# Kernel tuning notes

Hardware: AMD Instinct MI355X
Metric: run time of the kernel (lower is better)

## Reference

```python
import jax, jax.numpy as jnp
import numpy as np
import math

C = 256
N_HEAD = 8
GROUPS = 32
EPS = 1e-5


def group_norm(x, scale, bias, groups=GROUPS, eps=EPS):
    # x: [B, C, H, W]
    b, c, h, w = x.shape
    xg = x.reshape(b, groups, c // groups, h, w)
    mean = xg.mean(axis=(2, 3, 4), keepdims=True)
    var = xg.var(axis=(2, 3, 4), keepdims=True)
    xg = (xg - mean) * jax.lax.rsqrt(var + eps)
    x = xg.reshape(b, c, h, w)
    return x * scale[None, :, None, None] + bias[None, :, None, None]


def setup_inputs() -> dict:
    key = jax.random.key(0)
    ks = jax.random.split(key, 8)
    B, H, W = 8, 32, 32
    inp = {
        "input_q": jax.random.normal(ks[0], (B, C, H, W), dtype=jnp.float32),
        "input_kv": jax.random.normal(ks[1], (B, C, H, W), dtype=jnp.float32),
        # GroupNorm affine params (torch default: weight=1, bias=0)
        "gq_scale": jnp.ones((C,), jnp.float32),
        "gq_bias": jnp.zeros((C,), jnp.float32),
        "gkv_scale": jnp.ones((C,), jnp.float32),
        "gkv_bias": jnp.zeros((C,), jnp.float32),
        # 1x1 convs as [out, in] matrices
        "Wq": jax.random.normal(ks[2], (C, C), dtype=jnp.float32) / math.sqrt(C),
        "Wkv": jax.random.normal(ks[3], (2 * C, C), dtype=jnp.float32) / math.sqrt(C),
        "Wout": jax.random.normal(ks[4], (C, C), dtype=jnp.float32) / math.sqrt(C),
        "bout": jnp.zeros((C,), jnp.float32),
    }
    return inp


def reference(input_q, input_kv, gq_scale, gq_bias, gkv_scale, gkv_bias, Wq, Wkv, Wout, bout):
    b, c, h, w = input_q.shape
    n = N_HEAD
    d = c // n

    norm_q = group_norm(input_q, gq_scale, gq_bias)
    query = jnp.einsum('oc,bchw->bohw', Wq, norm_q).reshape(b, n, d, h, w)

    norm_kv = group_norm(input_kv, gkv_scale, gkv_bias)
    kv = jnp.einsum('oc,bchw->bohw', Wkv, norm_kv).reshape(b, n, 2 * d, h, w)
    key, value = kv[:, :, :d], kv[:, :, d:]

    attn = jnp.einsum('bnchw,bncyx->bnhwyx', query, key) / math.sqrt(c)
    attn = jax.nn.softmax(attn.reshape(b, n, h, w, h * w), axis=-1)
    attn = attn.reshape(b, n, h, w, h, w)

    out = jnp.einsum('bnhwyx,bncyx->bnchw', attn, value).reshape(b, c, h, w)
    out = jnp.einsum('oc,bchw->bohw', Wout, out) + bout[None, :, None, None]
    return out + input_q
```

## Files before the change

kernel.cpp:

```cpp
#include <hip/hip_runtime.h>
#include <hip/hip_bf16.h>
#include <math.h>
#include <string.h>

#define NB 8
#define NC 256
#define HWSZ 1024
#define NHEAD 8
#define DHEAD 32
#define NGRP 32
#define CPG 8
#define EPSV 1e-5f

typedef float f32x4 __attribute__((ext_vector_type(4)));
typedef short bf16x8 __attribute__((ext_vector_type(8)));

__device__ __forceinline__ unsigned pk2(float a, float b) {
    __hip_bfloat162 h = __float22bfloat162_rn(make_float2(a, b));
    unsigned r;
    memcpy(&r, &h, sizeof(r));
    return r;
}
__device__ __forceinline__ unsigned pk2t(float a, float b) {
    unsigned ua = __float_as_uint(a), ub = __float_as_uint(b);
    return (ua >> 16) | (ub & 0xFFFF0000u);
}
__device__ __forceinline__ unsigned short f2bf(float x) {
    __hip_bfloat16 h = __float2bfloat16(x);
    unsigned short r;
    memcpy(&r, &h, sizeof(r));
    return r;
}
__device__ __forceinline__ float ex2(float x) { return __builtin_amdgcn_exp2f(x); }

__device__ __forceinline__ void gload_lds16(const void* g, void* l) {
    __builtin_amdgcn_global_load_lds(
        (const __attribute__((address_space(1))) unsigned int*)g,
        (__attribute__((address_space(3))) unsigned int*)l, 16, 0, 0);
}

__global__ void prep_kernel(const float* __restrict__ xq,
                            const float* __restrict__ xkv,
                            float* __restrict__ stats,
                            const float* __restrict__ Wq,
                            const float* __restrict__ Wkv,
                            const float* __restrict__ Wout,
                            unsigned short* __restrict__ wqb,
                            unsigned short* __restrict__ wkvb,
                            unsigned short* __restrict__ woutb) {
    if (blockIdx.x < 512) {
        int idx = blockIdx.x;
        int which = idx >> 8;
        int b = (idx >> 5) & 7;
        int g = idx & 31;
        const float* x = which ? xkv : xq;
        const float4* xb = (const float4*)(x + ((size_t)(b * NC + g * CPG)) * HWSZ);
        float s = 0.f, ss = 0.f;
        for (int i = threadIdx.x; i < (CPG * HWSZ) / 4; i += 256) {
            float4 v = xb[i];
            s += v.x + v.y + v.z + v.w;
            ss += v.x * v.x + v.y * v.y + v.z * v.z + v.w * v.w;
        }
        #pragma unroll
        for (int off = 32; off > 0; off >>= 1) {
            s += __shfl_down(s, off);
            ss += __shfl_down(ss, off);
        }
        __shared__ float red[8];
        int wid = threadIdx.x >> 6;
        if ((threadIdx.x & 63) == 0) { red[wid * 2] = s; red[wid * 2 + 1] = ss; }
        __syncthreads();
        if (threadIdx.x == 0) {
            float S = red[0] + red[2] + red[4] + red[6];
            float SS = red[1] + red[3] + red[5] + red[7];
            float mean = S * (1.f / (CPG * HWSZ));
            float var = SS * (1.f / (CPG * HWSZ)) - mean * mean;
            stats[idx * 2] = mean;
            stats[idx * 2 + 1] = rsqrtf(var + EPSV);
        }
    } else {
        int gid = (blockIdx.x - 512) * 256 + threadIdx.x;
        int i0 = gid * 8;
        const float* src; unsigned short* dst; int off; float sc = 1.f;
        if (i0 < 65536)       { src = Wq;   dst = wqb;   off = i0;          sc = 0.0625f * 1.44269504088896f; }
        else if (i0 < 196608) { src = Wkv;  dst = wkvb;  off = i0 - 65536; }
        else                  { src = Wout; dst = woutb; off = i0 - 196608; }
        float4 v0 = *(const float4*)&src[off];
        float4 v1 = *(const float4*)&src[off + 4];
        uint4 o;
        o.x = pk2(v0.x * sc, v0.y * sc); o.y = pk2(v0.z * sc, v0.w * sc);
        o.z = pk2(v1.x * sc, v1.y * sc); o.w = pk2(v1.z * sc, v1.w * sc);
        *(uint4*)&dst[off] = o;
    }
}

__global__ __launch_bounds__(256) void qkv_gemm_kernel(
        const unsigned short* __restrict__ wqb,
        const unsigned short* __restrict__ wkvb,
        const float* __restrict__ xq, const float* __restrict__ xkv,
        const float* __restrict__ stats,
        const float* __restrict__ sq, const float* __restrict__ bq,
        const float* __restrict__ skv, const float* __restrict__ bkv,
        unsigned short* __restrict__ qbuf,
        unsigned short* __restrict__ kbuf,
        unsigned short* __restrict__ vbuf) {
    __shared__ unsigned short As[64 * 256];
    __shared__ unsigned short Bs[64 * 256];
    const int tid = threadIdx.x;
    const int l16 = tid & 15, g = (tid >> 4) & 3, w = tid >> 6;
    const int y = blockIdx.y;
    const bool isQ = y < 4;
    const int o0 = (isQ ? y : y - 4) * 64;
    const size_t prow0 = (size_t)blockIdx.x * 64;
    const int b = (int)(prow0 >> 10);
    const int pp = (int)(prow0 & 1023);

    const unsigned short* Asrc = (isQ ? wqb : wkvb) + (size_t)o0 * NC;
    const float* X  = (isQ ? xq : xkv) + (size_t)b * NC * HWSZ + pp;
    const float* st = stats + (isQ ? 0 : 512) + b * 64;
    const float* sc = isQ ? sq : skv;
    const float* bi = isQ ? bq : bkv;

    #pragma unroll
    for (int it = 0; it < 2; ++it) {
        int idx = tid + it * 256;
        int row = idx >> 3, seg2 = idx & 7;
        #pragma unroll
        for (int q4 = 0; q4 < 4; ++q4) {
            int seg = seg2 * 4 + q4;
            int ds = row * 256 + ((seg ^ (row & 7)) << 3);
            *(uint4*)&As[ds] = *(const uint4*)&Asrc[(size_t)row * NC + seg * 8];
        }
    }
    const int cq = tid >> 4, pq = tid & 15;
    #pragma unroll
    for (int j = 0; j < 4; ++j) {
        int cb = cq * 4 + j * 64;
        int grp = cb >> 3;
        float mean = st[grp * 2], rstd = st[grp * 2 + 1];
        float mm[4][4];
        #pragma unroll
        for (int u = 0; u < 4; ++u) {
            int c = cb + u;
            float4 v = *(const float4*)&X[(size_t)c * HWSZ + pq * 4];
            float a = rstd * sc[c];
            float bbv = bi[c] - mean * a;
            mm[u][0] = v.x * a + bbv; mm[u][1] = v.y * a + bbv;
            mm[u][2] = v.z * a + bbv; mm[u][3] = v.w * a + bbv;
        }
        #pragma unroll
        for (int v2 = 0; v2 < 4; ++v2) {
            int row = pq * 4 + v2;
            int ds = row * 256 + ((((cb >> 3) ^ (row & 7))) << 3) + (cb & 7);
            uint2 s2;
            s2.x = pk2(mm[0][v2], mm[1][v2]);
            s2.y = pk2(mm[2][v2], mm[3][v2]);
            *(uint2*)&Bs[ds] = s2;
        }
    }
    __syncthreads();

    f32x4 acc[4] = {};
    const int abase = (w * 16 + l16) * 256;
    const int asw = l16 & 7;
    #pragma unroll
    for (int kk = 0; kk < 8; ++kk) {
        const int koff = ((kk * 4 + g) ^ asw) << 3;
        bf16x8 a = *(const bf16x8*)&As[abase + koff];
        #pragma unroll
        for (int j = 0; j < 4; ++j) {
            bf16x8 bfr = *(const bf16x8*)&Bs[(j * 16 + l16) * 256 + koff];
            acc[j] = __builtin_amdgcn_mfma_f32_16x16x32_bf16(a, bfr, acc[j], 0, 0, 0);
        }
    }

    if (isQ) {
        int ob_ = o0 + 16 * w + 4 * g;
        int n = ob_ >> 5, d0 = ob_ & 31;
        unsigned short* dst = qbuf + ((size_t)(b * NHEAD + n) * HWSZ) * DHEAD + d0;
        #pragma unroll
        for (int j = 0; j < 4; ++j) {
            int p = pp + 16 * j + l16;
            uint2 st2;
            st2.x = pk2(acc[j][0], acc[j][1]);
            st2.y = pk2(acc[j][2], acc[j][3]);
            *(uint2*)&dst[(size_t)p * DHEAD] = st2;
        }
    } else {
        int n = o0 >> 6;
        int d0 = 16 * (w & 1) + 4 * g;
        if (w < 2) {
            unsigned short* dst = kbuf + ((size_t)(b * NHEAD + n) * HWSZ) * DHEAD + d0;
            #pragma unroll
            for (int j = 0; j < 4; ++j) {
                int p = pp + 16 * j + l16;
                uint2 st2;
                st2.x = pk2(acc[j][0], acc[j][1]);
                st2.y = pk2(acc[j][2], acc[j][3]);
                *(uint2*)&dst[(size_t)p * DHEAD] = st2;
            }
        } else {
            unsigned short* dst = vbuf + ((size_t)(b * NHEAD + n) * DHEAD + d0) * HWSZ;
            #pragma unroll
            for (int j = 0; j < 4; ++j) {
                int slot = ((l16 >> 2) << 3) + ((j & 1) << 2) + (l16 & 3);
                int p = pp + 32 * (j >> 1) + slot;
                #pragma unroll
                for (int r = 0; r < 4; ++r)
                    dst[(size_t)r * HWSZ + p] = f2bf(acc[j][r]);
            }
        }
    }
}

__global__ __launch_bounds__(256) void out_gemm_kernel(
        const unsigned short* __restrict__ Abase,
        const unsigned short* __restrict__ Bbase,
        const float* __restrict__ bias_out,
        const float* __restrict__ resid,
        float* __restrict__ out0) {
    __shared__ unsigned short As[64 * 256];
    __shared__ unsigned short Bs[64 * 256];
    const int tid = threadIdx.x;
    const int l16 = tid & 15, g = (tid >> 4) & 3, w = tid >> 6;
    const int o0 = blockIdx.y * 64;
    const size_t prow0 = (size_t)blockIdx.x * 64;
    const unsigned short* Asrc = Abase + prow0 * NC;
    const unsigned short* Bsrc = Bbase + (size_t)o0 * NC;
    #pragma unroll
    for (int it = 0; it < 8; ++it) {
        int idx = tid + it * 256;
        int row = idx >> 5, seg = idx & 31;
        int ds = row * 256 + ((seg ^ (row & 7)) << 3);
        *(uint4*)&As[ds] = *(const uint4*)&Asrc[(size_t)row * NC + seg * 8];
        *(uint4*)&Bs[ds] = *(const uint4*)&Bsrc[(size_t)row * NC + seg * 8];
    }
    __syncthreads();
    f32x4 acc[4] = {};
    const int abase = (w * 16 + l16) * 256;
    const int asw = l16 & 7;
    #pragma unroll
    for (int kk = 0; kk < 8; ++kk) {
        const int koff = ((kk * 4 + g) ^ asw) << 3;
        bf16x8 a = *(const bf16x8*)&As[abase + koff];
        #pragma unroll
        for (int j = 0; j < 4; ++j) {
            bf16x8 b = *(const bf16x8*)&Bs[(j * 16 + l16) * 256 + koff];
            acc[j] = __builtin_amdgcn_mfma_f32_16x16x32_bf16(a, b, acc[j], 0, 0, 0);
        }
    }
    const int b = (int)(prow0 >> 10);
    const int pp = (int)(prow0 & 1023);
    int p_b = pp + 16 * w + 4 * g;
    #pragma unroll
    for (int j = 0; j < 4; ++j) {
        int o = o0 + 16 * j + l16;
        float bo = bias_out[o];
        size_t off = ((size_t)b * NC + o) * HWSZ + p_b;
        float4 rs = *(const float4*)&resid[off];
        float4 vst = make_float4(acc[j][0] + bo + rs.x, acc[j][1] + bo + rs.y,
                                 acc[j][2] + bo + rs.z, acc[j][3] + bo + rs.w);
        *(float4*)&out0[off] = vst;
    }
}

__global__ __launch_bounds__(256) void attn_mfma_kernel(
        const unsigned short* __restrict__ qb,
        const unsigned short* __restrict__ kb,
        const unsigned short* __restrict__ vb,
        unsigned short* __restrict__ ob) {
    __shared__ unsigned short KV[3][4096];
    const int tid = threadIdx.x;
    const int w = tid >> 6, lane = tid & 63;
    const int l16 = lane & 15, g = lane >> 4;
    const int F = blockIdx.y * 16 + blockIdx.x;
    const int bn = (F & 7) * 8 + (F >> 7);
    const int qblk = (F >> 3) & 15;
    const int qp = qblk * 64 + w * 16 + l16;

    bf16x8 qf = *(const bf16x8*)(qb + ((size_t)bn * HWSZ + qp) * DHEAD + g * 8);

    const int kr = tid >> 2, ks = tid & 3;
    const unsigned short* ksrc = kb + (size_t)bn * HWSZ * DHEAD
                               + (size_t)kr * DHEAD + ((ks ^ (kr & 3)) << 3);
    const int vr = tid >> 3, vs = tid & 7;
    const unsigned short* vsrc = vb + (size_t)bn * DHEAD * HWSZ
                               + (size_t)vr * HWSZ + ((vs ^ (vr & 7)) << 3);
    unsigned short* lk = &KV[0][0] + w * 512;
    unsigned short* lv = &KV[0][2048] + w * 512;

#define STAGE(t) do {                                                        \
        int b3_ = (t) % 3; int ti_ = (t) & 15;                               \
        gload_lds16(ksrc + (size_t)ti_ * 64 * DHEAD, lk + b3_ * 4096);       \
        gload_lds16(vsrc + (size_t)ti_ * 64,         lv + b3_ * 4096);       \
    } while (0)

    f32x4 acc0 = {0.f, 0.f, 0.f, 0.f}, acc1 = {0.f, 0.f, 0.f, 0.f};
    float m = -INFINITY, l0 = 0.f, l1 = 0.f;
    const f32x4 z = {0.f, 0.f, 0.f, 0.f};

    const int ksw  = (g ^ (l16 & 3)) << 3;
    const int vsw0 = ((g)     ^ (l16 & 7)) << 3;
    const int vsw1 = ((4 + g) ^ (l16 & 7)) << 3;

    STAGE(0);
    STAGE(1);

    for (int t = 0; t < 16; ++t) {
        const int cur = t % 3;
        asm volatile("s_waitcnt vmcnt(2)" ::: "memory");
        __builtin_amdgcn_s_barrier();
        STAGE(t + 2);

        const unsigned short* Kb = &KV[cur][0];
        const unsigned short* Vb = &KV[cur][2048];
        bf16x8 ka0 = *(const bf16x8*)&Kb[(l16)      * 32 + ksw];
        bf16x8 ka1 = *(const bf16x8*)&Kb[(16 + l16) * 32 + ksw];
        bf16x8 ka2 = *(const bf16x8*)&Kb[(32 + l16) * 32 + ksw];
        bf16x8 ka3 = *(const bf16x8*)&Kb[(48 + l16) * 32 + ksw];

        f32x4 s0 = __builtin_amdgcn_mfma_f32_16x16x32_bf16(ka0, qf, z, 0, 0, 0);
        f32x4 s1 = __builtin_amdgcn_mfma_f32_16x16x32_bf16(ka1, qf, z, 0, 0, 0);
        f32x4 s2 = __builtin_amdgcn_mfma_f32_16x16x32_bf16(ka2, qf, z, 0, 0, 0);
        f32x4 s3 = __builtin_amdgcn_mfma_f32_16x16x32_bf16(ka3, qf, z, 0, 0, 0);

        float ta = fmaxf(fmaxf(fmaxf(s0[0], s0[1]), fmaxf(s0[2], s0[3])),
                         fmaxf(fmaxf(s1[0], s1[1]), fmaxf(s1[2], s1[3])));
        float tb = fmaxf(fmaxf(fmaxf(s2[0], s2[1]), fmaxf(s2[2], s2[3])),
                         fmaxf(fmaxf(s3[0], s3[1]), fmaxf(s3[2], s3[3])));
        float tm = fmaxf(ta, tb);
        if (!__all(tm <= m + 8.f)) {
            float tmr = fmaxf(tm, __shfl_xor(tm, 16, 64));
            tmr = fmaxf(tmr, __shfl_xor(tmr, 32, 64));
            float mnew = fmaxf(m, tmr);
            float corr = ex2(m - mnew);
            acc0 *= corr; acc1 *= corr; l0 *= corr; l1 *= corr;
            m = mnew;
        }
        float p00 = ex2(s0[0] - m), p01 = ex2(s0[1] - m);
        float p02 = ex2(s0[2] - m), p03 = ex2(s0[3] - m);
        float p10 = ex2(s1[0] - m), p11 = ex2(s1[1] - m);
        float p12 = ex2(s1[2] - m), p13 = ex2(s1[3] - m);
        float p20 = ex2(s2[0] - m), p21 = ex2(s2[1] - m);
        float p22 = ex2(s2[2] - m), p23 = ex2(s2[3] - m);
        float p30 = ex2(s3[0] - m), p31 = ex2(s3[1] - m);
        float p32 = ex2(s3[2] - m), p33 = ex2(s3[3] - m);
        l0 += ((p00 + p01) + (p02 + p03)) + ((p10 + p11) + (p12 + p13));
        l1 += ((p20 + p21) + (p22 + p23)) + ((p30 + p31) + (p32 + p33));

        uint4 pwa, pwb;
        pwa.x = pk2t(p00, p01); pwa.y = pk2t(p02, p03);
        pwa.z = pk2t(p10, p11); pwa.w = pk2t(p12, p13);
        pwb.x = pk2t(p20, p21); pwb.y = pk2t(p22, p23);
        pwb.z = pk2t(p30, p31); pwb.w = pk2t(p32, p33);
        bf16x8 pf0, pf1;
        memcpy(&pf0, &pwa, sizeof(pf0));
        memcpy(&pf1, &pwb, sizeof(pf1));

        bf16x8 va0 = *(const bf16x8*)&Vb[(l16)      * 64 + vsw0];
        bf16x8 va1 = *(const bf16x8*)&Vb[(l16)      * 64 + vsw1];
        bf16x8 vb0 = *(const bf16x8*)&Vb[(16 + l16) * 64 + vsw0];
        bf16x8 vb1 = *(const bf16x8*)&Vb[(16 + l16) * 64 + vsw1];

        acc0 = __builtin_amdgcn_mfma_f32_16x16x32_bf16(va0, pf0, acc0, 0, 0, 0);
        acc0 = __builtin_amdgcn_mfma_f32_16x16x32_bf16(va1, pf1, acc0, 0, 0, 0);
        acc1 = __builtin_amdgcn_mfma_f32_16x16x32_bf16(vb0, pf0, acc1, 0, 0, 0);
        acc1 = __builtin_amdgcn_mfma_f32_16x16x32_bf16(vb1, pf1, acc1, 0, 0, 0);
    }
#undef STAGE

    float l = l0 + l1;
    l += __shfl_xor(l, 16, 64);
    l += __shfl_xor(l, 32, 64);
    float invl = 1.f / l;

    const int b = bn >> 3, n = bn & 7;
    unsigned short* dst = ob + ((size_t)b * HWSZ + qp) * NC + n * DHEAD;
    uint2 st0, st1;
    st0.x = pk2(acc0[0] * invl, acc0[1] * invl);
    st0.y = pk2(acc0[2] * invl, acc0[3] * invl);
    st1.x = pk2(acc1[0] * invl, acc1[1] * invl);
    st1.y = pk2(acc1[2] * invl, acc1[3] * invl);
    *(uint2*)&dst[4 * g]      = st0;
    *(uint2*)&dst[16 + 4 * g] = st1;
}

extern "C" void kernel_launch(void* const* d_in, const int* in_sizes, int n_in,
                              void* d_out, int out_size, void* d_ws, size_t ws_size,
                              hipStream_t stream) {
    const float* input_q  = (const float*)d_in[0];
    const float* input_kv = (const float*)d_in[1];
    const float* gq_scale = (const float*)d_in[2];
    const float* gq_bias  = (const float*)d_in[3];
    const float* gkv_scale = (const float*)d_in[4];
    const float* gkv_bias  = (const float*)d_in[5];
    const float* Wq   = (const float*)d_in[6];
    const float* Wkv  = (const float*)d_in[7];
    const float* Wout = (const float*)d_in[8];
    const float* bout = (const float*)d_in[9];
    float* out = (float*)d_out;

    char* ws = (char*)d_ws;
    float* stats = (float*)ws;
    unsigned short* wqb   = (unsigned short*)(ws + 16384);
    unsigned short* wkvb  = (unsigned short*)(ws + 16384 + 131072);
    unsigned short* woutb = (unsigned short*)(ws + 16384 + 131072 + 262144);
    const size_t MB = 1024 * 1024;
    unsigned short* qbuf = (unsigned short*)(ws + 1 * MB);
    unsigned short* kbuf = (unsigned short*)(ws + 5 * MB);
    unsigned short* vbuf = (unsigned short*)(ws + 9 * MB);
    unsigned short* obuf = (unsigned short*)(ws + 13 * MB);

    prep_kernel<<<640, 256, 0, stream>>>(input_q, input_kv, stats,
                                         Wq, Wkv, Wout, wqb, wkvb, woutb);
    qkv_gemm_kernel<<<dim3(128, 12), 256, 0, stream>>>(
        wqb, wkvb, input_q, input_kv, stats,
        gq_scale, gq_bias, gkv_scale, gkv_bias, qbuf, kbuf, vbuf);
    attn_mfma_kernel<<<dim3(16, 64), 256, 0, stream>>>(qbuf, kbuf, vbuf, obuf);
    out_gemm_kernel<<<dim3(128, 4), 256, 0, stream>>>(obuf, woutb, bout, input_q, out);
}
```

Before: 54.09 us.

## Fold max subtraction into QK MFMA and compute row sums with ones-MFMA

Seeds the QK^T MFMA accumulator with the negated running max, so the subtraction before each exp2 is absorbed into the matrix op. The softmax denominator is now accumulated by extra MFMAs against a ones vector using the same bf16 P values, which replaces the scalar adds and cross-lane shuffles. The max-based rescaling becomes incremental and starts from a zero baseline. s_setprio hints are wrapped around the MFMA groups. This trades VALU work for two more MFMAs per tile, and the row sum is now taken from bf16-rounded P values.

New measurement: 51.97 us. -3.9%, faster.

```diff
diff --git a/kernel.cpp b/kernel.cpp
--- a/kernel.cpp
+++ b/kernel.cpp
@@ -296,8 +296,14 @@
     } while (0)
 
     f32x4 acc0 = {0.f, 0.f, 0.f, 0.f}, acc1 = {0.f, 0.f, 0.f, 0.f};
-    float m = -INFINITY, l0 = 0.f, l1 = 0.f;
-    const f32x4 z = {0.f, 0.f, 0.f, 0.f};
+    f32x4 accl = {0.f, 0.f, 0.f, 0.f};
+    float m = 0.f;
+    f32x4 mmv = {0.f, 0.f, 0.f, 0.f};
+
+    const unsigned on2 = 0x3F803F80u;
+    uint4 onev = make_uint4(on2, on2, on2, on2);
+    bf16x8 ones;
+    memcpy(&ones, &onev, sizeof(ones));
 
     const int ksw  = (g ^ (l16 & 3)) << 3;
     const int vsw0 = ((g)     ^ (l16 & 7)) << 3;
@@ -319,34 +325,40 @@
         bf16x8 ka2 = *(const bf16x8*)&Kb[(32 + l16) * 32 + ksw];
         bf16x8 ka3 = *(const bf16x8*)&Kb[(48 + l16) * 32 + ksw];
 
-        f32x4 s0 = __builtin_amdgcn_mfma_f32_16x16x32_bf16(ka0, qf, z, 0, 0, 0);
-        f32x4 s1 = __builtin_amdgcn_mfma_f32_16x16x32_bf16(ka1, qf, z, 0, 0, 0);
-        f32x4 s2 = __builtin_amdgcn_mfma_f32_16x16x32_bf16(ka2, qf, z, 0, 0, 0);
-        f32x4 s3 = __builtin_amdgcn_mfma_f32_16x16x32_bf16(ka3, qf, z, 0, 0, 0);
-
-        float ta = fmaxf(fmaxf(fmaxf(s0[0], s0[1]), fmaxf(s0[2], s0[3])),
-                         fmaxf(fmaxf(s1[0], s1[1]), fmaxf(s1[2], s1[3])));
-        float tb = fmaxf(fmaxf(fmaxf(s2[0], s2[1]), fmaxf(s2[2], s2[3])),
-                         fmaxf(fmaxf(s3[0], s3[1]), fmaxf(s3[2], s3[3])));
+        __builtin_amdgcn_s_setprio(1);
+        f32x4 s0 = __builtin_amdgcn_mfma_f32_16x16x32_bf16(ka0, qf, mmv, 0, 0, 0);
+        f32x4 s1 = __builtin_amdgcn_mfma_f32_16x16x32_bf16(ka1, qf, mmv, 0, 0, 0);
+        f32x4 s2 = __builtin_amdgcn_mfma_f32_16x16x32_bf16(ka2, qf, mmv, 0, 0, 0);
+        f32x4 s3 = __builtin_amdgcn_mfma_f32_16x16x32_bf16(ka3, qf, mmv, 0, 0, 0);
+        __builtin_amdgcn_s_setprio(0);
+
+        float ta = fmaxf(fmaxf(s0[0], s0[1]), s0[2]);
+        ta = fmaxf(fmaxf(ta, s0[3]), s1[0]);
+        ta = fmaxf(fmaxf(ta, s1[1]), s1[2]);
+        ta = fmaxf(ta, s1[3]);
+        float tb = fmaxf(fmaxf(s2[0], s2[1]), s2[2]);
+        tb = fmaxf(fmaxf(tb, s2[3]), s3[0]);
+        tb = fmaxf(fmaxf(tb, s3[1]), s3[2]);
+        tb = fmaxf(tb, s3[3]);
         float tm = fmaxf(ta, tb);
-        if (!__all(tm <= m + 8.f)) {
+        if (!__all(tm <= 8.f)) {
             float tmr = fmaxf(tm, __shfl_xor(tm, 16, 64));
             tmr = fmaxf(tmr, __shfl_xor(tmr, 32, 64));
-            float mnew = fmaxf(m, tmr);
-            float corr = ex2(m - mnew);
-            acc0 *= corr; acc1 *= corr; l0 *= corr; l1 *= corr;
-            m = mnew;
-        }
-        float p00 = ex2(s0[0] - m), p01 = ex2(s0[1] - m);
-        float p02 = ex2(s0[2] - m), p03 = ex2(s0[3] - m);
-        float p10 = ex2(s1[0] - m), p11 = ex2(s1[1] - m);
-        float p12 = ex2(s1[2] - m), p13 = ex2(s1[3] - m);
-        float p20 = ex2(s2[0] - m), p21 = ex2(s2[1] - m);
-        float p22 = ex2(s2[2] - m), p23 = ex2(s2[3] - m);
-        float p30 = ex2(s3[0] - m), p31 = ex2(s3[1] - m);
-        float p32 = ex2(s3[2] - m), p33 = ex2(s3[3] - m);
-        l0 += ((p00 + p01) + (p02 + p03)) + ((p10 + p11) + (p12 + p13));
-        l1 += ((p20 + p21) + (p22 + p23)) + ((p30 + p31) + (p32 + p33));
+            float inc = fmaxf(tmr, 0.f);
+            float corr = ex2(-inc);
+            acc0 *= corr; acc1 *= corr; accl *= corr;
+            m += inc;
+            mmv[0] = -m; mmv[1] = -m; mmv[2] = -m; mmv[3] = -m;
+            s0 -= inc; s1 -= inc; s2 -= inc; s3 -= inc;
+        }
+        float p00 = ex2(s0[0]), p01 = ex2(s0[1]);
+        float p02 = ex2(s0[2]), p03 = ex2(s0[3]);
+        float p10 = ex2(s1[0]), p11 = ex2(s1[1]);
+        float p12 = ex2(s1[2]), p13 = ex2(s1[3]);
+        float p20 = ex2(s2[0]), p21 = ex2(s2[1]);
+        float p22 = ex2(s2[2]), p23 = ex2(s2[3]);
+        float p30 = ex2(s3[0]), p31 = ex2(s3[1]);
+        float p32 = ex2(s3[2]), p33 = ex2(s3[3]);
 
         uint4 pwa, pwb;
         pwa.x = pk2t(p00, p01); pwa.y = pk2t(p02, p03);
@@ -362,17 +374,18 @@
         bf16x8 vb0 = *(const bf16x8*)&Vb[(16 + l16) * 64 + vsw0];
         bf16x8 vb1 = *(const bf16x8*)&Vb[(16 + l16) * 64 + vsw1];
 
+        __builtin_amdgcn_s_setprio(1);
         acc0 = __builtin_amdgcn_mfma_f32_16x16x32_bf16(va0, pf0, acc0, 0, 0, 0);
         acc0 = __builtin_amdgcn_mfma_f32_16x16x32_bf16(va1, pf1, acc0, 0, 0, 0);
         acc1 = __builtin_amdgcn_mfma_f32_16x16x32_bf16(vb0, pf0, acc1, 0, 0, 0);
         acc1 = __builtin_amdgcn_mfma_f32_16x16x32_bf16(vb1, pf1, acc1, 0, 0, 0);
+        accl = __builtin_amdgcn_mfma_f32_16x16x32_bf16(ones, pf0, accl, 0, 0, 0);
+        accl = __builtin_amdgcn_mfma_f32_16x16x32_bf16(ones, pf1, accl, 0, 0, 0);
+        __builtin_amdgcn_s_setprio(0);
     }
 #undef STAGE
 
-    float l = l0 + l1;
-    l += __shfl_xor(l, 16, 64);
-    l += __shfl_xor(l, 32, 64);
-    float invl = 1.f / l;
+    float invl = 1.f / accl[0];
 
     const int b = bn >> 3, n = bn & 7;
     unsigned short* dst = ob + ((size_t)b * HWSZ + qp) * NC + n * DHEAD;
```
